# Performance work log

Measured on AMD Instinct MI355X. Metric: run time of the kernel, lower is better.

The kernel has to match this reference:

```python
import jax, jax.numpy as jnp
import numpy as np

E, K, H, I, T = 32, 4, 1024, 1024, 1024
ALPHA, BETA = 1.702, 1.0  # swiglu_alpha, swiglu_beta from the module


def setup_inputs() -> dict:
    key = jax.random.key(0)
    k0, k1, k2, k3 = jax.random.split(key, 4)
    return {
        "hidden_states": jax.random.normal(k0, (T, H), jnp.float32),
        "gate_w": jax.random.normal(k1, (H, E), jnp.float32) * (H ** -0.5),
        "gate_b": jnp.zeros((E,), jnp.float32),
        # pair_wise_act=True: gate/up are interleaved along the last dim of w1's output
        "w1": jax.random.normal(k2, (E, H, 2 * I), jnp.float32) * (H ** -0.5),
        "b1": jnp.zeros((E, 2 * I), jnp.float32),
        "w2": jax.random.normal(k3, (E, I, H), jnp.float32) * (I ** -0.5),
        "b2": jnp.zeros((E, H), jnp.float32),
    }


def reference(hidden_states, gate_w, gate_b, w1, b1, w2, b2):
    # Router gate (ReplicatedLinear with bias)
    router_logits = hidden_states @ gate_w + gate_b            # [T, E]
    probs = jax.nn.softmax(router_logits, axis=-1)
    topk_w, topk_idx = jax.lax.top_k(probs, K)                 # [T, K]
    # renormalize (norm_topk_prob=True)
    topk_w = topk_w / jnp.sum(topk_w, axis=-1, keepdims=True)
    # combine weights per (expert, token): sum over slots where idx == e
    onehot = (topk_idx[None, :, :] == jnp.arange(E)[:, None, None])  # [E, T, K]
    combine_w = jnp.sum(onehot * topk_w[None, :, :], axis=-1)        # [E, T]
    # Expert MLPs (grouped GEMM expressed as dense-per-expert einsum)
    h = jnp.einsum('th,ehd->etd', hidden_states, w1) + b1[:, None, :]  # [E, T, 2I]
    gate = h[..., 0::2]   # interleaved pairwise gate
    up = h[..., 1::2]     # interleaved pairwise up
    act = (up + BETA) * gate * jax.nn.sigmoid(ALPHA * gate)           # [E, T, I]
    y = jnp.einsum('eti,eih->eth', act, w2) + b2[:, None, :]          # [E, T, H]
    # weighted combine across selected experts
    return jnp.einsum('eth,et->th', y, combine_w)                     # [T, H]
```

## Files before the change

kernel.cpp:

```cpp
#include <hip/hip_runtime.h>
#include <hip/hip_bf16.h>
#include <math.h>

#define E_ 32
#define K_ 4
#define H_ 1024
#define I_ 1024
#define T_ 1024
#define TWO_I 2048

typedef __attribute__((ext_vector_type(4))) float float4v;
typedef __attribute__((ext_vector_type(8))) short short8v;
typedef __attribute__((ext_vector_type(4))) short short4v;

__device__ __forceinline__ unsigned short f2bf(float f) {
    unsigned u = __float_as_uint(f);
    u = (u + 0x7FFFu + ((u >> 16) & 1u)) >> 16;
    return (unsigned short)u;
}
__device__ __forceinline__ short4v cvt4(float4v v) {
    union { unsigned u[2]; short4v s; } r;
    asm("v_cvt_pk_bf16_f32 %0, %1, %2" : "=v"(r.u[0]) : "v"(v[0]), "v"(v[1]));
    asm("v_cvt_pk_bf16_f32 %0, %1, %2" : "=v"(r.u[1]) : "v"(v[2]), "v"(v[3]));
    return r.s;
}
__device__ __forceinline__ int permpos(int k4) {
    return ((k4 >> 5) << 5) + (((k4 >> 2) & 3) << 3) + (((k4 >> 4) & 1) << 2);
}

__global__ __launch_bounds__(256) void hs2bf_kernel(
    const float* __restrict__ hs, unsigned short* __restrict__ hsb) {
    int i = blockIdx.x * 256 + threadIdx.x;
    float4v v = *(const float4v*)(hs + (size_t)i * 4);
    *(short4v*)(hsb + (size_t)i * 4) = cvt4(v);
}

__global__ __launch_bounds__(256) void router_kernel(
    const float* __restrict__ hs, const float* __restrict__ gw,
    const float* __restrict__ gb, int* __restrict__ counts,
    int* __restrict__ token_list, float* __restrict__ weight_list) {
    int wv = threadIdx.x >> 6, lane = threadIdx.x & 63;
    int t = blockIdx.x * 4 + wv;
    int e = lane & 31;
    int half = lane >> 5;
    const float* hrow = hs + (size_t)t * H_;
    const float* gcol = gw + e;
    float a0 = 0.f, a1 = 0.f;
    int hb = half * 512;
#pragma unroll 4
    for (int h = 0; h < 512; h += 2) {
        a0 = fmaf(hrow[hb + h],     gcol[(size_t)(hb + h) * E_], a0);
        a1 = fmaf(hrow[hb + h + 1], gcol[(size_t)(hb + h + 1) * E_], a1);
    }
    float part = a0 + a1;
    part += __shfl_xor(part, 32);
    float cur = part + gb[e];

    int idx4[K_]; float val4[K_];
#pragma unroll
    for (int k = 0; k < K_; ++k) {
        float m = cur;
#pragma unroll
        for (int d = 1; d < 64; d <<= 1) m = fmaxf(m, __shfl_xor(m, d));
        unsigned long long b = __ballot(cur == m);
        int l = __ffsll(b) - 1;
        idx4[k] = l & 31; val4[k] = m;
        if (e == (l & 31)) cur = -INFINITY;
    }
    float mx = val4[0], s = 0.f, wv4[K_];
#pragma unroll
    for (int k = 0; k < K_; ++k) { wv4[k] = expf(val4[k] - mx); s += wv4[k]; }
    float inv = 1.f / s;
    if (lane < K_) {
        int ex = idx4[lane];
        int slot = atomicAdd(&counts[ex], 1);
        token_list[ex * T_ + slot] = t;
        weight_list[ex * T_ + slot] = wv4[lane] * inv;
    }
}

#define G_COMPUTE(BUF)                                                         \
    _Pragma("unroll")                                                          \
    for (int s = 0; s < 2; ++s) {                                              \
        short8v afr[4];                                                        \
        _Pragma("unroll")                                                      \
        for (int mi = 0; mi < 4; ++mi) {                                       \
            int row = wm * 64 + mi * 16 + l15;                                 \
            afr[mi] = *(const short8v*)&As[BUF][row * 64 + ((s * 32 + g * 8) ^ sw)]; \
        }                                                                      \
        short4v bl[2], bh[2];                                                  \
        _Pragma("unroll")                                                      \
        for (int ni = 0; ni < 2; ++ni) {                                       \
            unsigned ad = ((BUF) ? trb1 : trb0) + (unsigned)(ni * 2048 + s * 1024); \
            asm volatile("ds_read_b64_tr_b16 %0, %1" : "=v"(bl[ni]) : "v"(ad));     \
            asm volatile("ds_read_b64_tr_b16 %0, %1" : "=v"(bh[ni]) : "v"(ad + 512u)); \
        }                                                                      \
        asm volatile("s_waitcnt lgkmcnt(0)" ::: "memory");                     \
        __builtin_amdgcn_sched_barrier(0);                                     \
        _Pragma("unroll")                                                      \
        for (int ni = 0; ni < 2; ++ni) {                                       \
            short8v b;                                                         \
            b[0] = bl[ni][0]; b[1] = bl[ni][1]; b[2] = bl[ni][2]; b[3] = bl[ni][3]; \
            b[4] = bh[ni][0]; b[5] = bh[ni][1]; b[6] = bh[ni][2]; b[7] = bh[ni][3]; \
            _Pragma("unroll")                                                  \
            for (int mi = 0; mi < 4; ++mi)                                     \
                acc[mi][ni] = __builtin_amdgcn_mfma_f32_16x16x32_bf16(afr[mi], b, acc[mi][ni], 0, 0, 0); \
        }                                                                      \
    }

#define G_STEP(BUF, KN, BSTRIDE, ISLAST)                                       \
    {                                                                          \
        __syncthreads();                                                       \
        if (!(ISLAST)) {                                                       \
            _Pragma("unroll")                                                  \
            for (int i = 0; i < 4; ++i)                                        \
                ra[i] = aptr[i] ? *(const short8v*)(aptr[i] + (KN)) : z8;      \
            _Pragma("unroll")                                                  \
            for (int i = 0; i < 4; ++i)                                        \
                rb[i] = *(const float4v*)(bptrB + (size_t)(KN) * (BSTRIDE) + (size_t)(i * 16) * (BSTRIDE)); \
        }                                                                      \
        __builtin_amdgcn_sched_barrier(0);                                     \
        G_COMPUTE(BUF)                                                         \
        if (!(ISLAST)) {                                                       \
            _Pragma("unroll")                                                  \
            for (int i = 0; i < 4; ++i) {                                      \
                short8v v = ra[i];                                             \
                short4v lo, hi;                                                \
                lo[0] = v[0]; lo[1] = v[1]; lo[2] = v[2]; lo[3] = v[3];        \
                hi[0] = v[4]; hi[1] = v[5]; hi[2] = v[6]; hi[3] = v[7];        \
                *(short4v*)&As[(BUF) ^ 1][aw0[i]] = lo;                        \
                *(short4v*)&As[(BUF) ^ 1][aw1[i]] = hi;                        \
            }                                                                  \
            _Pragma("unroll")                                                  \
            for (int i = 0; i < 4; ++i) *(short4v*)&Bs[(BUF) ^ 1][bwidx[i]] = cvt4(rb[i]); \
        }                                                                      \
    }

__global__ __launch_bounds__(256, 3) void gemm1_kernel(
    const unsigned short* __restrict__ hsb, const float* __restrict__ w1,
    const float* __restrict__ b1, const int* __restrict__ counts,
    const int* __restrict__ token_list, unsigned short* __restrict__ actb) {
    int e = blockIdx.z;
    int cnt = counts[e];
    int m0 = blockIdx.y * 128;
    if (m0 >= cnt) return;
    int cb = blockIdx.x * 64;
    const float* w1e = w1 + (size_t)e * H_ * TWO_I;
    const int* tl = token_list + e * T_;

    __shared__ __align__(16) short As[2][128 * 64];
    __shared__ __align__(16) short Bs[2][64 * 64];

    int tid = threadIdx.x;
    int lane = tid & 63;
    int wid = tid >> 6;
    int wm = wid >> 1, wn = wid & 1;
    int g = lane >> 4;
    int l15 = lane & 15;
    int sw = (l15 & 7) << 3;
    unsigned trb0 = (unsigned)(size_t)(&Bs[0][0]) + (unsigned)(lane * 8) + (unsigned)(wn * 4096);
    unsigned trb1 = (unsigned)(size_t)(&Bs[1][0]) + (unsigned)(lane * 8) + (unsigned)(wn * 4096);

    int q = tid & 7;
    const unsigned short* aptr[4]; int aw0[4], aw1[4];
#pragma unroll
    for (int i = 0; i < 4; ++i) {
        int row = i * 32 + (tid >> 3);
        int gr = m0 + row;
        aptr[i] = (gr < cnt) ? hsb + (size_t)tl[gr] * H_ + q * 8 : nullptr;
        int swr = (row & 7) << 3;
        aw0[i] = row * 64 + (permpos(q * 8) ^ swr);
        aw1[i] = row * 64 + (permpos(q * 8 + 4) ^ swr);
    }
    int c4 = (tid & 15) << 2;
    const float* bptrB = w1e + (size_t)(tid >> 4) * TWO_I + cb + c4;
    int bwidx[4];
#pragma unroll
    for (int i = 0; i < 4; ++i) {
        int krow = i * 16 + (tid >> 4);
        bwidx[i] = ((c4 >> 4) * 16 + (krow >> 2)) * 64 + (krow & 3) * 16 + (c4 & 15);
    }

    float4v acc[4][2];
#pragma unroll
    for (int i = 0; i < 4; ++i)
#pragma unroll
        for (int j = 0; j < 2; ++j) acc[i][j] = (float4v){0.f, 0.f, 0.f, 0.f};

    short8v ra[4]; float4v rb[4];
    const short8v z8 = {0, 0, 0, 0, 0, 0, 0, 0};
#pragma unroll
    for (int i = 0; i < 4; ++i) ra[i] = aptr[i] ? *(const short8v*)(aptr[i]) : z8;
#pragma unroll
    for (int i = 0; i < 4; ++i) rb[i] = *(const float4v*)(bptrB + (size_t)(i * 16) * TWO_I);
#pragma unroll
    for (int i = 0; i < 4; ++i) {
        short8v v = ra[i];
        short4v lo, hi;
        lo[0] = v[0]; lo[1] = v[1]; lo[2] = v[2]; lo[3] = v[3];
        hi[0] = v[4]; hi[1] = v[5]; hi[2] = v[6]; hi[3] = v[7];
        *(short4v*)&As[0][aw0[i]] = lo;
        *(short4v*)&As[0][aw1[i]] = hi;
    }
#pragma unroll
    for (int i = 0; i < 4; ++i) *(short4v*)&Bs[0][bwidx[i]] = cvt4(rb[i]);

#pragma unroll 1
    for (int kk = 0; kk < H_; kk += 128) {
        G_STEP(0, kk + 64, TWO_I, false)
        G_STEP(1, kk + 128, TWO_I, (kk + 128) >= H_)
    }

    const float* b1e = b1 + (size_t)e * TWO_I;
#pragma unroll
    for (int mi = 0; mi < 4; ++mi) {
#pragma unroll
        for (int r = 0; r < 4; ++r) {
            int gm = m0 + wm * 64 + mi * 16 + g * 4 + r;
#pragma unroll
            for (int ni = 0; ni < 2; ++ni) {
                float v = acc[mi][ni][r];
                float o = __shfl_xor(v, 1);
                if (!(lane & 1) && gm < cnt) {
                    int wc = cb + wn * 32 + ni * 16 + l15;
                    float gate = v + b1e[wc];
                    float up   = o + b1e[wc + 1];
                    float sg = 1.f / (1.f + __expf(-1.702f * gate));
                    float av = (up + 1.f) * gate * sg;
                    actb[(size_t)(e * T_ + gm) * I_ + (wc >> 1)] = f2bf(av);
                }
            }
        }
    }
}

__global__ __launch_bounds__(256, 3) void gemm2_kernel(
    const unsigned short* __restrict__ actb, const float* __restrict__ w2,
    const float* __restrict__ b2, const int* __restrict__ counts,
    const int* __restrict__ token_list, const float* __restrict__ weight_list,
    float* __restrict__ out) {
    int e = blockIdx.z;
    int cnt = counts[e];
    int m0 = blockIdx.y * 128;
    if (m0 >= cnt) return;
    int h0 = (blockIdx.x >> 1) * 64;
    int kbase = (blockIdx.x & 1) * 512;
    const float* w2e = w2 + (size_t)e * I_ * H_;
    const int* tl = token_list + e * T_;

    __shared__ __align__(16) short As[2][128 * 64];
    __shared__ __align__(16) short Bs[2][64 * 64];

    int tid = threadIdx.x;
    int lane = tid & 63;
    int wid = tid >> 6;
    int wm = wid >> 1, wn = wid & 1;
    int g = lane >> 4;
    int l15 = lane & 15;
    int sw = (l15 & 7) << 3;
    unsigned trb0 = (unsigned)(size_t)(&Bs[0][0]) + (unsigned)(lane * 8) + (unsigned)(wn * 4096);
    unsigned trb1 = (unsigned)(size_t)(&Bs[1][0]) + (unsigned)(lane * 8) + (unsigned)(wn * 4096);

    int q = tid & 7;
    const unsigned short* aptr[4]; int aw0[4], aw1[4];
#pragma unroll
    for (int i = 0; i < 4; ++i) {
        int row = i * 32 + (tid >> 3);
        int gr = m0 + row;
        aptr[i] = (gr < cnt) ? actb + (size_t)(e * T_ + gr) * I_ + kbase + q * 8 : nullptr;
        int swr = (row & 7) << 3;
        aw0[i] = row * 64 + (permpos(q * 8) ^ swr);
        aw1[i] = row * 64 + (permpos(q * 8 + 4) ^ swr);
    }
    int c4 = (tid & 15) << 2;
    const float* bptrB = w2e + (size_t)(kbase + (tid >> 4)) * H_ + h0 + c4;
    int bwidx[4];
#pragma unroll
    for (int i = 0; i < 4; ++i) {
        int krow = i * 16 + (tid >> 4);
        bwidx[i] = ((c4 >> 4) * 16 + (krow >> 2)) * 64 + (krow & 3) * 16 + (c4 & 15);
    }

    float4v acc[4][2];
#pragma unroll
    for (int i = 0; i < 4; ++i)
#pragma unroll
        for (int j = 0; j < 2; ++j) acc[i][j] = (float4v){0.f, 0.f, 0.f, 0.f};

    short8v ra[4]; float4v rb[4];
    const short8v z8 = {0, 0, 0, 0, 0, 0, 0, 0};
#pragma unroll
    for (int i = 0; i < 4; ++i) ra[i] = aptr[i] ? *(const short8v*)(aptr[i]) : z8;
#pragma unroll
    for (int i = 0; i < 4; ++i) rb[i] = *(const float4v*)(bptrB + (size_t)(i * 16) * H_);
#pragma unroll
    for (int i = 0; i < 4; ++i) {
        short8v v = ra[i];
        short4v lo, hi;
        lo[0] = v[0]; lo[1] = v[1]; lo[2] = v[2]; lo[3] = v[3];
        hi[0] = v[4]; hi[1] = v[5]; hi[2] = v[6]; hi[3] = v[7];
        *(short4v*)&As[0][aw0[i]] = lo;
        *(short4v*)&As[0][aw1[i]] = hi;
    }
#pragma unroll
    for (int i = 0; i < 4; ++i) *(short4v*)&Bs[0][bwidx[i]] = cvt4(rb[i]);

#pragma unroll 1
    for (int kk = 0; kk < 512; kk += 128) {
        G_STEP(0, kk + 64, H_, false)
        G_STEP(1, kk + 128, H_, (kk + 128) >= 512)
    }

    const float* b2e = b2 + (size_t)e * H_;
    const float* wl = weight_list + e * T_;
    bool addbias = (kbase == 0);
#pragma unroll
    for (int mi = 0; mi < 4; ++mi) {
#pragma unroll
        for (int r = 0; r < 4; ++r) {
            int gm = m0 + wm * 64 + mi * 16 + g * 4 + r;
            if (gm < cnt) {
                int t = tl[gm];
                float wgt = wl[gm];
#pragma unroll
                for (int ni = 0; ni < 2; ++ni) {
                    int h = h0 + wn * 32 + ni * 16 + l15;
                    float v = acc[mi][ni][r];
                    if (addbias) v += b2e[h];
                    atomicAdd(&out[(size_t)t * H_ + h], v * wgt);
                }
            }
        }
    }
}

extern "C" void kernel_launch(void* const* d_in, const int* in_sizes, int n_in,
                              void* d_out, int out_size, void* d_ws, size_t ws_size,
                              hipStream_t stream) {
    const float* hs = (const float*)d_in[0];
    const float* gw = (const float*)d_in[1];
    const float* gb = (const float*)d_in[2];
    const float* w1 = (const float*)d_in[3];
    const float* b1 = (const float*)d_in[4];
    const float* w2 = (const float*)d_in[5];
    const float* b2 = (const float*)d_in[6];
    float* out = (float*)d_out;

    char* ws = (char*)d_ws;
    int*   counts      = (int*)ws;
    int*   token_list  = (int*)(ws + 4096);
    float* weight_list = (float*)(ws + 4096 + 131072);
    unsigned short* hsb  = (unsigned short*)(ws + (1 << 20));
    unsigned short* actb = (unsigned short*)(ws + (1 << 20) + (2 << 20));

    hipMemsetAsync(counts, 0, 32 * sizeof(int), stream);
    hipMemsetAsync(d_out, 0, (size_t)out_size * sizeof(float), stream);

    hs2bf_kernel<<<(T_ * H_ / 4) / 256, 256, 0, stream>>>(hs, hsb);
    router_kernel<<<T_ / 4, 256, 0, stream>>>(hs, gw, gb, counts, token_list, weight_list);
    gemm1_kernel<<<dim3(TWO_I / 64, T_ / 128, E_), 256, 0, stream>>>(
        hsb, w1, b1, counts, token_list, actb);
    gemm2_kernel<<<dim3((H_ / 64) * 2, T_ / 128, E_), 256, 0, stream>>>(
        actb, w2, b2, counts, token_list, weight_list, out);
}
```

Baseline: 203.9 us.

## Deepen global prefetch to two stages and fold memsets into prep kernel

Both grouped GEMM kernels now keep two register sets for prefetched A/B tiles, so global loads are issued two k-steps ahead instead of one, hiding more memory latency. The output zeroing and counts reset, previously done with two hipMemsetAsync calls, are folded into the bf16 conversion kernel, which removes two launches. The extra prefetch registers raise register pressure, which may cut occupancy under the 3-blocks-per-SM launch bound.

Result: slower. 262.0 us (+28.5%).

```diff
diff --git a/kernel.cpp b/kernel.cpp
--- a/kernel.cpp
+++ b/kernel.cpp
@@ -28,11 +28,14 @@
     return ((k4 >> 5) << 5) + (((k4 >> 2) & 3) << 3) + (((k4 >> 4) & 1) << 2);
 }
 
-__global__ __launch_bounds__(256) void hs2bf_kernel(
-    const float* __restrict__ hs, unsigned short* __restrict__ hsb) {
+__global__ __launch_bounds__(256) void prep_kernel(
+    const float* __restrict__ hs, unsigned short* __restrict__ hsb,
+    float* __restrict__ out, int* __restrict__ counts) {
     int i = blockIdx.x * 256 + threadIdx.x;
     float4v v = *(const float4v*)(hs + (size_t)i * 4);
     *(short4v*)(hsb + (size_t)i * 4) = cvt4(v);
+    *(float4v*)(out + (size_t)i * 4) = (float4v){0.f, 0.f, 0.f, 0.f};
+    if (blockIdx.x == 0 && threadIdx.x < E_) counts[threadIdx.x] = 0;
 }
 
 __global__ __launch_bounds__(256) void router_kernel(
@@ -108,23 +111,23 @@
         }                                                                      \
     }
 
-#define G_STEP(BUF, KN, BSTRIDE, ISLAST)                                       \
+#define G_STEP3(BUF, RAI, RBI, RAW, RBW, KN, BSTRIDE, DOISS, DOWR)             \
     {                                                                          \
         __syncthreads();                                                       \
-        if (!(ISLAST)) {                                                       \
+        if (DOISS) {                                                           \
             _Pragma("unroll")                                                  \
             for (int i = 0; i < 4; ++i)                                        \
-                ra[i] = aptr[i] ? *(const short8v*)(aptr[i] + (KN)) : z8;      \
+                RAI[i] = aptr[i] ? *(const short8v*)(aptr[i] + (KN)) : z8;     \
             _Pragma("unroll")                                                  \
             for (int i = 0; i < 4; ++i)                                        \
-                rb[i] = *(const float4v*)(bptrB + (size_t)(KN) * (BSTRIDE) + (size_t)(i * 16) * (BSTRIDE)); \
+                RBI[i] = *(const float4v*)(bptrB + (size_t)(KN) * (BSTRIDE) + (size_t)(i * 16) * (BSTRIDE)); \
         }                                                                      \
         __builtin_amdgcn_sched_barrier(0);                                     \
         G_COMPUTE(BUF)                                                         \
-        if (!(ISLAST)) {                                                       \
+        if (DOWR) {                                                            \
             _Pragma("unroll")                                                  \
             for (int i = 0; i < 4; ++i) {                                      \
-                short8v v = ra[i];                                             \
+                short8v v = RAW[i];                                            \
                 short4v lo, hi;                                                \
                 lo[0] = v[0]; lo[1] = v[1]; lo[2] = v[2]; lo[3] = v[3];        \
                 hi[0] = v[4]; hi[1] = v[5]; hi[2] = v[6]; hi[3] = v[7];        \
@@ -132,7 +135,7 @@
                 *(short4v*)&As[(BUF) ^ 1][aw1[i]] = hi;                        \
             }                                                                  \
             _Pragma("unroll")                                                  \
-            for (int i = 0; i < 4; ++i) *(short4v*)&Bs[(BUF) ^ 1][bwidx[i]] = cvt4(rb[i]); \
+            for (int i = 0; i < 4; ++i) *(short4v*)&Bs[(BUF) ^ 1][bwidx[i]] = cvt4(RBW[i]); \
         }                                                                      \
     }
 
@@ -187,15 +190,15 @@
 #pragma unroll
         for (int j = 0; j < 2; ++j) acc[i][j] = (float4v){0.f, 0.f, 0.f, 0.f};
 
-    short8v ra[4]; float4v rb[4];
+    short8v raA[4], raB[4]; float4v rbA[4], rbB[4];
     const short8v z8 = {0, 0, 0, 0, 0, 0, 0, 0};
 #pragma unroll
-    for (int i = 0; i < 4; ++i) ra[i] = aptr[i] ? *(const short8v*)(aptr[i]) : z8;
-#pragma unroll
-    for (int i = 0; i < 4; ++i) rb[i] = *(const float4v*)(bptrB + (size_t)(i * 16) * TWO_I);
-#pragma unroll
-    for (int i = 0; i < 4; ++i) {
-        short8v v = ra[i];
+    for (int i = 0; i < 4; ++i) raA[i] = aptr[i] ? *(const short8v*)(aptr[i]) : z8;
+#pragma unroll
+    for (int i = 0; i < 4; ++i) rbA[i] = *(const float4v*)(bptrB + (size_t)(i * 16) * TWO_I);
+#pragma unroll
+    for (int i = 0; i < 4; ++i) {
+        short8v v = raA[i];
         short4v lo, hi;
         lo[0] = v[0]; lo[1] = v[1]; lo[2] = v[2]; lo[3] = v[3];
         hi[0] = v[4]; hi[1] = v[5]; hi[2] = v[6]; hi[3] = v[7];
@@ -203,12 +206,16 @@
         *(short4v*)&As[0][aw1[i]] = hi;
     }
 #pragma unroll
-    for (int i = 0; i < 4; ++i) *(short4v*)&Bs[0][bwidx[i]] = cvt4(rb[i]);
+    for (int i = 0; i < 4; ++i) *(short4v*)&Bs[0][bwidx[i]] = cvt4(rbA[i]);
+#pragma unroll
+    for (int i = 0; i < 4; ++i) raB[i] = aptr[i] ? *(const short8v*)(aptr[i] + 64) : z8;
+#pragma unroll
+    for (int i = 0; i < 4; ++i) rbB[i] = *(const float4v*)(bptrB + (size_t)64 * TWO_I + (size_t)(i * 16) * TWO_I);
 
 #pragma unroll 1
     for (int kk = 0; kk < H_; kk += 128) {
-        G_STEP(0, kk + 64, TWO_I, false)
-        G_STEP(1, kk + 128, TWO_I, (kk + 128) >= H_)
+        G_STEP3(0, raA, rbA, raB, rbB, kk + 128, TWO_I, (kk + 128) < H_, true)
+        G_STEP3(1, raB, rbB, raA, rbA, kk + 192, TWO_I, (kk + 192) < H_, (kk + 128) < H_)
     }
 
     const float* b1e = b1 + (size_t)e * TWO_I;
@@ -287,15 +294,15 @@
 #pragma unroll
         for (int j = 0; j < 2; ++j) acc[i][j] = (float4v){0.f, 0.f, 0.f, 0.f};
 
-    short8v ra[4]; float4v rb[4];
+    short8v raA[4], raB[4]; float4v rbA[4], rbB[4];
     const short8v z8 = {0, 0, 0, 0, 0, 0, 0, 0};
 #pragma unroll
-    for (int i = 0; i < 4; ++i) ra[i] = aptr[i] ? *(const short8v*)(aptr[i]) : z8;
-#pragma unroll
-    for (int i = 0; i < 4; ++i) rb[i] = *(const float4v*)(bptrB + (size_t)(i * 16) * H_);
-#pragma unroll
-    for (int i = 0; i < 4; ++i) {
-        short8v v = ra[i];
+    for (int i = 0; i < 4; ++i) raA[i] = aptr[i] ? *(const short8v*)(aptr[i]) : z8;
+#pragma unroll
+    for (int i = 0; i < 4; ++i) rbA[i] = *(const float4v*)(bptrB + (size_t)(i * 16) * H_);
+#pragma unroll
+    for (int i = 0; i < 4; ++i) {
+        short8v v = raA[i];
         short4v lo, hi;
         lo[0] = v[0]; lo[1] = v[1]; lo[2] = v[2]; lo[3] = v[3];
         hi[0] = v[4]; hi[1] = v[5]; hi[2] = v[6]; hi[3] = v[7];
@@ -303,12 +310,16 @@
         *(short4v*)&As[0][aw1[i]] = hi;
     }
 #pragma unroll
-    for (int i = 0; i < 4; ++i) *(short4v*)&Bs[0][bwidx[i]] = cvt4(rb[i]);
+    for (int i = 0; i < 4; ++i) *(short4v*)&Bs[0][bwidx[i]] = cvt4(rbA[i]);
+#pragma unroll
+    for (int i = 0; i < 4; ++i) raB[i] = aptr[i] ? *(const short8v*)(aptr[i] + 64) : z8;
+#pragma unroll
+    for (int i = 0; i < 4; ++i) rbB[i] = *(const float4v*)(bptrB + (size_t)64 * H_ + (size_t)(i * 16) * H_);
 
 #pragma unroll 1
     for (int kk = 0; kk < 512; kk += 128) {
-        G_STEP(0, kk + 64, H_, false)
-        G_STEP(1, kk + 128, H_, (kk + 128) >= 512)
+        G_STEP3(0, raA, rbA, raB, rbB, kk + 128, H_, (kk + 128) < 512, true)
+        G_STEP3(1, raB, rbB, raA, rbA, kk + 192, H_, (kk + 192) < 512, (kk + 128) < 512)
     }
 
     const float* b2e = b2 + (size_t)e * H_;
@@ -353,10 +364,7 @@
     unsigned short* hsb  = (unsigned short*)(ws + (1 << 20));
     unsigned short* actb = (unsigned short*)(ws + (1 << 20) + (2 << 20));
 
-    hipMemsetAsync(counts, 0, 32 * sizeof(int), stream);
-    hipMemsetAsync(d_out, 0, (size_t)out_size * sizeof(float), stream);
-
-    hs2bf_kernel<<<(T_ * H_ / 4) / 256, 256, 0, stream>>>(hs, hsb);
+    prep_kernel<<<(T_ * H_ / 4) / 256, 256, 0, stream>>>(hs, hsb, out, counts);
     router_kernel<<<T_ / 4, 256, 0, stream>>>(hs, gw, gb, counts, token_list, weight_list);
     gemm1_kernel<<<dim3(TWO_I / 64, T_ / 128, E_), 256, 0, stream>>>(
         hsb, w1, b1, counts, token_list, actb);
```

## Read A operand directly from global memory, drop A LDS staging, fuse memsets

Applied to the files above, without the earlier changes.

Both grouped GEMM kernels stop staging the A tile (gathered tokens or activations) through shared memory. Each lane now loads its MFMA A fragments straight from global memory through per-row pointers, and out-of-range rows are clamped to the last valid row. This frees LDS so occupancy can rise to 5 blocks, and the K loop is restructured into single 64-wide steps. The two memsets are folded into the bf16 conversion kernel, which removes launch overhead. The risk is that A is now read uncoalesced and redundantly from global/L2 memory, once per wave column, instead of once per block.

Result: slower. 397.9 us (+95.2%).

```diff
diff --git a/kernel.cpp b/kernel.cpp
--- a/kernel.cpp
+++ b/kernel.cpp
@@ -24,15 +24,15 @@
     asm("v_cvt_pk_bf16_f32 %0, %1, %2" : "=v"(r.u[1]) : "v"(v[2]), "v"(v[3]));
     return r.s;
 }
-__device__ __forceinline__ int permpos(int k4) {
-    return ((k4 >> 5) << 5) + (((k4 >> 2) & 3) << 3) + (((k4 >> 4) & 1) << 2);
-}
-
-__global__ __launch_bounds__(256) void hs2bf_kernel(
-    const float* __restrict__ hs, unsigned short* __restrict__ hsb) {
+
+__global__ __launch_bounds__(256) void prep_kernel(
+    const float* __restrict__ hs, unsigned short* __restrict__ hsb,
+    float* __restrict__ out, int* __restrict__ counts) {
     int i = blockIdx.x * 256 + threadIdx.x;
     float4v v = *(const float4v*)(hs + (size_t)i * 4);
     *(short4v*)(hsb + (size_t)i * 4) = cvt4(v);
+    *(float4v*)(out + (size_t)i * 4) = (float4v){0.f, 0.f, 0.f, 0.f};
+    if (blockIdx.x == 0 && threadIdx.x < E_) counts[threadIdx.x] = 0;
 }
 
 __global__ __launch_bounds__(256) void router_kernel(
@@ -79,14 +79,18 @@
     }
 }
 
-#define G_COMPUTE(BUF)                                                         \
+#define G_COMPUTE(BUF, KK)                                                     \
     _Pragma("unroll")                                                          \
     for (int s = 0; s < 2; ++s) {                                              \
         short8v afr[4];                                                        \
         _Pragma("unroll")                                                      \
         for (int mi = 0; mi < 4; ++mi) {                                       \
-            int row = wm * 64 + mi * 16 + l15;                                 \
-            afr[mi] = *(const short8v*)&As[BUF][row * 64 + ((s * 32 + g * 8) ^ sw)]; \
+            short4v alo = *(const short4v*)(rp[mi] + (KK) + s * 32 + 4 * g);   \
+            short4v ahi = *(const short4v*)(rp[mi] + (KK) + s * 32 + 16 + 4 * g); \
+            short8v a;                                                         \
+            a[0] = alo[0]; a[1] = alo[1]; a[2] = alo[2]; a[3] = alo[3];        \
+            a[4] = ahi[0]; a[5] = ahi[1]; a[6] = ahi[2]; a[7] = ahi[3];        \
+            afr[mi] = a;                                                       \
         }                                                                      \
         short4v bl[2], bh[2];                                                  \
         _Pragma("unroll")                                                      \
@@ -108,35 +112,7 @@
         }                                                                      \
     }
 
-#define G_STEP(BUF, KN, BSTRIDE, ISLAST)                                       \
-    {                                                                          \
-        __syncthreads();                                                       \
-        if (!(ISLAST)) {                                                       \
-            _Pragma("unroll")                                                  \
-            for (int i = 0; i < 4; ++i)                                        \
-                ra[i] = aptr[i] ? *(const short8v*)(aptr[i] + (KN)) : z8;      \
-            _Pragma("unroll")                                                  \
-            for (int i = 0; i < 4; ++i)                                        \
-                rb[i] = *(const float4v*)(bptrB + (size_t)(KN) * (BSTRIDE) + (size_t)(i * 16) * (BSTRIDE)); \
-        }                                                                      \
-        __builtin_amdgcn_sched_barrier(0);                                     \
-        G_COMPUTE(BUF)                                                         \
-        if (!(ISLAST)) {                                                       \
-            _Pragma("unroll")                                                  \
-            for (int i = 0; i < 4; ++i) {                                      \
-                short8v v = ra[i];                                             \
-                short4v lo, hi;                                                \
-                lo[0] = v[0]; lo[1] = v[1]; lo[2] = v[2]; lo[3] = v[3];        \
-                hi[0] = v[4]; hi[1] = v[5]; hi[2] = v[6]; hi[3] = v[7];        \
-                *(short4v*)&As[(BUF) ^ 1][aw0[i]] = lo;                        \
-                *(short4v*)&As[(BUF) ^ 1][aw1[i]] = hi;                        \
-            }                                                                  \
-            _Pragma("unroll")                                                  \
-            for (int i = 0; i < 4; ++i) *(short4v*)&Bs[(BUF) ^ 1][bwidx[i]] = cvt4(rb[i]); \
-        }                                                                      \
-    }
-
-__global__ __launch_bounds__(256, 3) void gemm1_kernel(
+__global__ __launch_bounds__(256, 5) void gemm1_kernel(
     const unsigned short* __restrict__ hsb, const float* __restrict__ w1,
     const float* __restrict__ b1, const int* __restrict__ counts,
     const int* __restrict__ token_list, unsigned short* __restrict__ actb) {
@@ -148,7 +124,6 @@
     const float* w1e = w1 + (size_t)e * H_ * TWO_I;
     const int* tl = token_list + e * T_;
 
-    __shared__ __align__(16) short As[2][128 * 64];
     __shared__ __align__(16) short Bs[2][64 * 64];
 
     int tid = threadIdx.x;
@@ -157,20 +132,15 @@
     int wm = wid >> 1, wn = wid & 1;
     int g = lane >> 4;
     int l15 = lane & 15;
-    int sw = (l15 & 7) << 3;
     unsigned trb0 = (unsigned)(size_t)(&Bs[0][0]) + (unsigned)(lane * 8) + (unsigned)(wn * 4096);
-    unsigned trb1 = (unsigned)(size_t)(&Bs[1][0]) + (unsigned)(lane * 8) + (unsigned)(wn * 4096);
-
-    int q = tid & 7;
-    const unsigned short* aptr[4]; int aw0[4], aw1[4];
-#pragma unroll
-    for (int i = 0; i < 4; ++i) {
-        int row = i * 32 + (tid >> 3);
-        int gr = m0 + row;
-        aptr[i] = (gr < cnt) ? hsb + (size_t)tl[gr] * H_ + q * 8 : nullptr;
-        int swr = (row & 7) << 3;
-        aw0[i] = row * 64 + (permpos(q * 8) ^ swr);
-        aw1[i] = row * 64 + (permpos(q * 8 + 4) ^ swr);
+    unsigned trb1 = trb0 + 8192u;
+
+    const unsigned short* rp[4];
+#pragma unroll
+    for (int mi = 0; mi < 4; ++mi) {
+        int gr = m0 + wm * 64 + mi * 16 + l15;
+        int gi = (gr < cnt) ? gr : (cnt - 1);
+        rp[mi] = hsb + (size_t)tl[gi] * H_;
     }
     int c4 = (tid & 15) << 2;
     const float* bptrB = w1e + (size_t)(tid >> 4) * TWO_I + cb + c4;
@@ -187,28 +157,26 @@
 #pragma unroll
         for (int j = 0; j < 2; ++j) acc[i][j] = (float4v){0.f, 0.f, 0.f, 0.f};
 
-    short8v ra[4]; float4v rb[4];
-    const short8v z8 = {0, 0, 0, 0, 0, 0, 0, 0};
-#pragma unroll
-    for (int i = 0; i < 4; ++i) ra[i] = aptr[i] ? *(const short8v*)(aptr[i]) : z8;
+    float4v rb[4];
 #pragma unroll
     for (int i = 0; i < 4; ++i) rb[i] = *(const float4v*)(bptrB + (size_t)(i * 16) * TWO_I);
 #pragma unroll
-    for (int i = 0; i < 4; ++i) {
-        short8v v = ra[i];
-        short4v lo, hi;
-        lo[0] = v[0]; lo[1] = v[1]; lo[2] = v[2]; lo[3] = v[3];
-        hi[0] = v[4]; hi[1] = v[5]; hi[2] = v[6]; hi[3] = v[7];
-        *(short4v*)&As[0][aw0[i]] = lo;
-        *(short4v*)&As[0][aw1[i]] = hi;
-    }
-#pragma unroll
     for (int i = 0; i < 4; ++i) *(short4v*)&Bs[0][bwidx[i]] = cvt4(rb[i]);
 
 #pragma unroll 1
-    for (int kk = 0; kk < H_; kk += 128) {
-        G_STEP(0, kk + 64, TWO_I, false)
-        G_STEP(1, kk + 128, TWO_I, (kk + 128) >= H_)
+    for (int kk = 0; kk < H_; kk += 64) {
+        int buf = (kk >> 6) & 1;
+        __syncthreads();
+        if (kk + 64 < H_) {
+#pragma unroll
+            for (int i = 0; i < 4; ++i)
+                rb[i] = *(const float4v*)(bptrB + (size_t)(kk + 64) * TWO_I + (size_t)(i * 16) * TWO_I);
+        }
+        G_COMPUTE(buf, kk)
+        if (kk + 64 < H_) {
+#pragma unroll
+            for (int i = 0; i < 4; ++i) *(short4v*)&Bs[buf ^ 1][bwidx[i]] = cvt4(rb[i]);
+        }
     }
 
     const float* b1e = b1 + (size_t)e * TWO_I;
@@ -234,7 +202,7 @@
     }
 }
 
-__global__ __launch_bounds__(256, 3) void gemm2_kernel(
+__global__ __launch_bounds__(256, 5) void gemm2_kernel(
     const unsigned short* __restrict__ actb, const float* __restrict__ w2,
     const float* __restrict__ b2, const int* __restrict__ counts,
     const int* __restrict__ token_list, const float* __restrict__ weight_list,
@@ -248,7 +216,6 @@
     const float* w2e = w2 + (size_t)e * I_ * H_;
     const int* tl = token_list + e * T_;
 
-    __shared__ __align__(16) short As[2][128 * 64];
     __shared__ __align__(16) short Bs[2][64 * 64];
 
     int tid = threadIdx.x;
@@ -257,20 +224,15 @@
     int wm = wid >> 1, wn = wid & 1;
     int g = lane >> 4;
     int l15 = lane & 15;
-    int sw = (l15 & 7) << 3;
     unsigned trb0 = (unsigned)(size_t)(&Bs[0][0]) + (unsigned)(lane * 8) + (unsigned)(wn * 4096);
-    unsigned trb1 = (unsigned)(size_t)(&Bs[1][0]) + (unsigned)(lane * 8) + (unsigned)(wn * 4096);
-
-    int q = tid & 7;
-    const unsigned short* aptr[4]; int aw0[4], aw1[4];
-#pragma unroll
-    for (int i = 0; i < 4; ++i) {
-        int row = i * 32 + (tid >> 3);
-        int gr = m0 + row;
-        aptr[i] = (gr < cnt) ? actb + (size_t)(e * T_ + gr) * I_ + kbase + q * 8 : nullptr;
-        int swr = (row & 7) << 3;
-        aw0[i] = row * 64 + (permpos(q * 8) ^ swr);
-        aw1[i] = row * 64 + (permpos(q * 8 + 4) ^ swr);
+    unsigned trb1 = trb0 + 8192u;
+
+    const unsigned short* rp[4];
+#pragma unroll
+    for (int mi = 0; mi < 4; ++mi) {
+        int gr = m0 + wm * 64 + mi * 16 + l15;
+        int gi = (gr < cnt) ? gr : (cnt - 1);
+        rp[mi] = actb + (size_t)(e * T_ + gi) * I_ + kbase;
     }
     int c4 = (tid & 15) << 2;
     const float* bptrB = w2e + (size_t)(kbase + (tid >> 4)) * H_ + h0 + c4;
@@ -287,28 +249,26 @@
 #pragma unroll
         for (int j = 0; j < 2; ++j) acc[i][j] = (float4v){0.f, 0.f, 0.f, 0.f};
 
-    short8v ra[4]; float4v rb[4];
-    const short8v z8 = {0, 0, 0, 0, 0, 0, 0, 0};
-#pragma unroll
-    for (int i = 0; i < 4; ++i) ra[i] = aptr[i] ? *(const short8v*)(aptr[i]) : z8;
+    float4v rb[4];
 #pragma unroll
     for (int i = 0; i < 4; ++i) rb[i] = *(const float4v*)(bptrB + (size_t)(i * 16) * H_);
 #pragma unroll
-    for (int i = 0; i < 4; ++i) {
-        short8v v = ra[i];
-        short4v lo, hi;
-        lo[0] = v[0]; lo[1] = v[1]; lo[2] = v[2]; lo[3] = v[3];
-        hi[0] = v[4]; hi[1] = v[5]; hi[2] = v[6]; hi[3] = v[7];
-        *(short4v*)&As[0][aw0[i]] = lo;
-        *(short4v*)&As[0][aw1[i]] = hi;
-    }
-#pragma unroll
     for (int i = 0; i < 4; ++i) *(short4v*)&Bs[0][bwidx[i]] = cvt4(rb[i]);
 
 #pragma unroll 1
-    for (int kk = 0; kk < 512; kk += 128) {
-        G_STEP(0, kk + 64, H_, false)
-        G_STEP(1, kk + 128, H_, (kk + 128) >= 512)
+    for (int kk = 0; kk < 512; kk += 64) {
+        int buf = (kk >> 6) & 1;
+        __syncthreads();
+        if (kk + 64 < 512) {
+#pragma unroll
+            for (int i = 0; i < 4; ++i)
+                rb[i] = *(const float4v*)(bptrB + (size_t)(kk + 64) * H_ + (size_t)(i * 16) * H_);
+        }
+        G_COMPUTE(buf, kk)
+        if (kk + 64 < 512) {
+#pragma unroll
+            for (int i = 0; i < 4; ++i) *(short4v*)&Bs[buf ^ 1][bwidx[i]] = cvt4(rb[i]);
+        }
     }
 
     const float* b2e = b2 + (size_t)e * H_;
@@ -353,10 +313,7 @@
     unsigned short* hsb  = (unsigned short*)(ws + (1 << 20));
     unsigned short* actb = (unsigned short*)(ws + (1 << 20) + (2 << 20));
 
-    hipMemsetAsync(counts, 0, 32 * sizeof(int), stream);
-    hipMemsetAsync(d_out, 0, (size_t)out_size * sizeof(float), stream);
-
-    hs2bf_kernel<<<(T_ * H_ / 4) / 256, 256, 0, stream>>>(hs, hsb);
+    prep_kernel<<<(T_ * H_ / 4) / 256, 256, 0, stream>>>(hs, hsb, out, counts);
     router_kernel<<<T_ / 4, 256, 0, stream>>>(hs, gw, gb, counts, token_list, weight_list);
     gemm1_kernel<<<dim3(TWO_I / 64, T_ / 128, E_), 256, 0, stream>>>(
         hsb, w1, b1, counts, token_list, actb);
```

## Halve gemm1 M tile to 64 rows and fold memsets into prep kernel

Applied to the files above, without the earlier changes.

The gemm1 block tile drops from 128 to 64 token rows, and the launch bound rises to 5 blocks per CU, so per-expert token counts near 128 waste less padded work and the grid gains occupancy. The compute and step macros now take the A-load count, M-fragment count and row base as parameters so gemm1 and gemm2 can use different tile heights. Separately, the output zeroing and the expert counter reset move into the bf16 conversion kernel, which removes two memset calls. The cost is that each fp32 w1 column tile is now loaded and converted by more blocks per expert, which raises weight traffic unless it hits in L2.

Result: no change. 202.8 us (-0.5%).

```diff
diff --git a/kernel.cpp b/kernel.cpp
--- a/kernel.cpp
+++ b/kernel.cpp
@@ -28,11 +28,14 @@
     return ((k4 >> 5) << 5) + (((k4 >> 2) & 3) << 3) + (((k4 >> 4) & 1) << 2);
 }
 
-__global__ __launch_bounds__(256) void hs2bf_kernel(
-    const float* __restrict__ hs, unsigned short* __restrict__ hsb) {
+__global__ __launch_bounds__(256) void prep_kernel(
+    const float* __restrict__ hs, unsigned short* __restrict__ hsb,
+    float* __restrict__ out, int* __restrict__ counts) {
     int i = blockIdx.x * 256 + threadIdx.x;
     float4v v = *(const float4v*)(hs + (size_t)i * 4);
     *(short4v*)(hsb + (size_t)i * 4) = cvt4(v);
+    *(float4v*)(out + (size_t)i * 4) = (float4v){0.f, 0.f, 0.f, 0.f};
+    if (blockIdx.x == 0 && threadIdx.x < E_) counts[threadIdx.x] = 0;
 }
 
 __global__ __launch_bounds__(256) void router_kernel(
@@ -79,13 +82,13 @@
     }
 }
 
-#define G_COMPUTE(BUF)                                                         \
+#define G_COMPUTE(BUF, NM, ROWBASE)                                            \
     _Pragma("unroll")                                                          \
     for (int s = 0; s < 2; ++s) {                                              \
-        short8v afr[4];                                                        \
+        short8v afr[NM];                                                       \
         _Pragma("unroll")                                                      \
-        for (int mi = 0; mi < 4; ++mi) {                                       \
-            int row = wm * 64 + mi * 16 + l15;                                 \
+        for (int mi = 0; mi < NM; ++mi) {                                      \
+            int row = (ROWBASE) + mi * 16 + l15;                               \
             afr[mi] = *(const short8v*)&As[BUF][row * 64 + ((s * 32 + g * 8) ^ sw)]; \
         }                                                                      \
         short4v bl[2], bh[2];                                                  \
@@ -103,27 +106,27 @@
             b[0] = bl[ni][0]; b[1] = bl[ni][1]; b[2] = bl[ni][2]; b[3] = bl[ni][3]; \
             b[4] = bh[ni][0]; b[5] = bh[ni][1]; b[6] = bh[ni][2]; b[7] = bh[ni][3]; \
             _Pragma("unroll")                                                  \
-            for (int mi = 0; mi < 4; ++mi)                                     \
+            for (int mi = 0; mi < NM; ++mi)                                    \
                 acc[mi][ni] = __builtin_amdgcn_mfma_f32_16x16x32_bf16(afr[mi], b, acc[mi][ni], 0, 0, 0); \
         }                                                                      \
     }
 
-#define G_STEP(BUF, KN, BSTRIDE, ISLAST)                                       \
+#define G_STEP(BUF, KN, BSTRIDE, ISLAST, NA, NM, ROWBASE)                      \
     {                                                                          \
         __syncthreads();                                                       \
         if (!(ISLAST)) {                                                       \
             _Pragma("unroll")                                                  \
-            for (int i = 0; i < 4; ++i)                                        \
+            for (int i = 0; i < NA; ++i)                                       \
                 ra[i] = aptr[i] ? *(const short8v*)(aptr[i] + (KN)) : z8;      \
             _Pragma("unroll")                                                  \
             for (int i = 0; i < 4; ++i)                                        \
                 rb[i] = *(const float4v*)(bptrB + (size_t)(KN) * (BSTRIDE) + (size_t)(i * 16) * (BSTRIDE)); \
         }                                                                      \
         __builtin_amdgcn_sched_barrier(0);                                     \
-        G_COMPUTE(BUF)                                                         \
+        G_COMPUTE(BUF, NM, ROWBASE)                                            \
         if (!(ISLAST)) {                                                       \
             _Pragma("unroll")                                                  \
-            for (int i = 0; i < 4; ++i) {                                      \
+            for (int i = 0; i < NA; ++i) {                                     \
                 short8v v = ra[i];                                             \
                 short4v lo, hi;                                                \
                 lo[0] = v[0]; lo[1] = v[1]; lo[2] = v[2]; lo[3] = v[3];        \
@@ -136,19 +139,19 @@
         }                                                                      \
     }
 
-__global__ __launch_bounds__(256, 3) void gemm1_kernel(
+__global__ __launch_bounds__(256, 5) void gemm1_kernel(
     const unsigned short* __restrict__ hsb, const float* __restrict__ w1,
     const float* __restrict__ b1, const int* __restrict__ counts,
     const int* __restrict__ token_list, unsigned short* __restrict__ actb) {
     int e = blockIdx.z;
     int cnt = counts[e];
-    int m0 = blockIdx.y * 128;
+    int m0 = blockIdx.y * 64;
     if (m0 >= cnt) return;
     int cb = blockIdx.x * 64;
     const float* w1e = w1 + (size_t)e * H_ * TWO_I;
     const int* tl = token_list + e * T_;
 
-    __shared__ __align__(16) short As[2][128 * 64];
+    __shared__ __align__(16) short As[2][64 * 64];
     __shared__ __align__(16) short Bs[2][64 * 64];
 
     int tid = threadIdx.x;
@@ -162,9 +165,9 @@
     unsigned trb1 = (unsigned)(size_t)(&Bs[1][0]) + (unsigned)(lane * 8) + (unsigned)(wn * 4096);
 
     int q = tid & 7;
-    const unsigned short* aptr[4]; int aw0[4], aw1[4];
-#pragma unroll
-    for (int i = 0; i < 4; ++i) {
+    const unsigned short* aptr[2]; int aw0[2], aw1[2];
+#pragma unroll
+    for (int i = 0; i < 2; ++i) {
         int row = i * 32 + (tid >> 3);
         int gr = m0 + row;
         aptr[i] = (gr < cnt) ? hsb + (size_t)tl[gr] * H_ + q * 8 : nullptr;
@@ -181,20 +184,20 @@
         bwidx[i] = ((c4 >> 4) * 16 + (krow >> 2)) * 64 + (krow & 3) * 16 + (c4 & 15);
     }
 
-    float4v acc[4][2];
-#pragma unroll
-    for (int i = 0; i < 4; ++i)
+    float4v acc[2][2];
+#pragma unroll
+    for (int i = 0; i < 2; ++i)
 #pragma unroll
         for (int j = 0; j < 2; ++j) acc[i][j] = (float4v){0.f, 0.f, 0.f, 0.f};
 
-    short8v ra[4]; float4v rb[4];
+    short8v ra[2]; float4v rb[4];
     const short8v z8 = {0, 0, 0, 0, 0, 0, 0, 0};
 #pragma unroll
-    for (int i = 0; i < 4; ++i) ra[i] = aptr[i] ? *(const short8v*)(aptr[i]) : z8;
+    for (int i = 0; i < 2; ++i) ra[i] = aptr[i] ? *(const short8v*)(aptr[i]) : z8;
 #pragma unroll
     for (int i = 0; i < 4; ++i) rb[i] = *(const float4v*)(bptrB + (size_t)(i * 16) * TWO_I);
 #pragma unroll
-    for (int i = 0; i < 4; ++i) {
+    for (int i = 0; i < 2; ++i) {
         short8v v = ra[i];
         short4v lo, hi;
         lo[0] = v[0]; lo[1] = v[1]; lo[2] = v[2]; lo[3] = v[3];
@@ -207,16 +210,16 @@
 
 #pragma unroll 1
     for (int kk = 0; kk < H_; kk += 128) {
-        G_STEP(0, kk + 64, TWO_I, false)
-        G_STEP(1, kk + 128, TWO_I, (kk + 128) >= H_)
+        G_STEP(0, kk + 64, TWO_I, false, 2, 2, wm * 32)
+        G_STEP(1, kk + 128, TWO_I, (kk + 128) >= H_, 2, 2, wm * 32)
     }
 
     const float* b1e = b1 + (size_t)e * TWO_I;
 #pragma unroll
-    for (int mi = 0; mi < 4; ++mi) {
+    for (int mi = 0; mi < 2; ++mi) {
 #pragma unroll
         for (int r = 0; r < 4; ++r) {
-            int gm = m0 + wm * 64 + mi * 16 + g * 4 + r;
+            int gm = m0 + wm * 32 + mi * 16 + g * 4 + r;
 #pragma unroll
             for (int ni = 0; ni < 2; ++ni) {
                 float v = acc[mi][ni][r];
@@ -307,8 +310,8 @@
 
 #pragma unroll 1
     for (int kk = 0; kk < 512; kk += 128) {
-        G_STEP(0, kk + 64, H_, false)
-        G_STEP(1, kk + 128, H_, (kk + 128) >= 512)
+        G_STEP(0, kk + 64, H_, false, 4, 4, wm * 64)
+        G_STEP(1, kk + 128, H_, (kk + 128) >= 512, 4, 4, wm * 64)
     }
 
     const float* b2e = b2 + (size_t)e * H_;
@@ -353,12 +356,9 @@
     unsigned short* hsb  = (unsigned short*)(ws + (1 << 20));
     unsigned short* actb = (unsigned short*)(ws + (1 << 20) + (2 << 20));
 
-    hipMemsetAsync(counts, 0, 32 * sizeof(int), stream);
-    hipMemsetAsync(d_out, 0, (size_t)out_size * sizeof(float), stream);
-
-    hs2bf_kernel<<<(T_ * H_ / 4) / 256, 256, 0, stream>>>(hs, hsb);
+    prep_kernel<<<(T_ * H_ / 4) / 256, 256, 0, stream>>>(hs, hsb, out, counts);
     router_kernel<<<T_ / 4, 256, 0, stream>>>(hs, gw, gb, counts, token_list, weight_list);
-    gemm1_kernel<<<dim3(TWO_I / 64, T_ / 128, E_), 256, 0, stream>>>(
+    gemm1_kernel<<<dim3(TWO_I / 64, T_ / 64, E_), 256, 0, stream>>>(
         hsb, w1, b1, counts, token_list, actb);
     gemm2_kernel<<<dim3((H_ / 64) * 2, T_ / 128, E_), 256, 0, stream>>>(
         actb, w2, b2, counts, token_list, weight_list, out);
```
